# Kernel tuning notes

Measured on AMD Instinct MI355X. Metric: run time of the kernel, lower is better.

The kernel has to match this reference:

```python
import jax, jax.numpy as jnp
import numpy as np

N, E, G = 16384, 131072, 64
IN_DIM, HID, HEADS, GDIM, OUT_DIM = 256, 128, 4, 2, 2


def _glorot(key, shape):
    fan_in = shape[0]
    return jax.random.normal(key, shape, dtype=jnp.float32) / jnp.sqrt(jnp.float32(fan_in))


def gatv2_layer(x, src, dst, Wl, bl, Wr, br, att, bias, heads, ch, concat):
    """GATv2Conv: e_ij = att . leaky_relu(Wl x_j + Wr x_i, 0.2), segment softmax over dst."""
    n = x.shape[0]
    xl = (x @ Wl + bl).reshape(n, heads, ch)  # source transform
    xr = (x @ Wr + br).reshape(n, heads, ch)  # target transform
    h = jax.nn.leaky_relu(xl[src] + xr[dst], 0.2)          # [E', H, C]
    e = jnp.einsum('ehc,hc->eh', h, att)                   # [E', H]
    m = jax.ops.segment_max(e, dst, num_segments=n)        # stable softmax per target
    p = jnp.exp(e - m[dst])
    denom = jax.ops.segment_sum(p, dst, num_segments=n)
    alpha = p / denom[dst]                                 # self-loops guarantee denom>0
    out = jax.ops.segment_sum(alpha[..., None] * xl[src], dst, num_segments=n)  # [n,H,C]
    out = out.reshape(n, heads * ch) if concat else out.mean(axis=1)
    return out + bias


def setup_inputs() -> dict:
    key = jax.random.key(0)
    ks = jax.random.split(key, 24)
    inp = {
        'x': jax.random.normal(ks[0], (N, IN_DIM), dtype=jnp.float32),
        'edge_index': jax.random.randint(ks[1], (2, E), 0, N, dtype=jnp.int64)
            if jax.config.jax_enable_x64 else jax.random.randint(ks[1], (2, E), 0, N).astype(jnp.int32),
        'batch': jnp.sort(jax.random.randint(ks[2], (N,), 0, G)).astype(jnp.int32),
        'global_features': jax.random.normal(ks[3], (G, GDIM), dtype=jnp.float32),
    }
    # conv1: in=256 -> heads*hid=512 (concat)
    inp['c1_Wl'] = _glorot(ks[4], (IN_DIM, HEADS * HID)); inp['c1_bl'] = jnp.zeros((HEADS * HID,), jnp.float32)
    inp['c1_Wr'] = _glorot(ks[5], (IN_DIM, HEADS * HID)); inp['c1_br'] = jnp.zeros((HEADS * HID,), jnp.float32)
    inp['c1_att'] = _glorot(ks[6], (HEADS, HID)); inp['c1_bias'] = jnp.zeros((HEADS * HID,), jnp.float32)
    # conv2: in=512 -> 512 (concat)
    D2 = HEADS * HID
    inp['c2_Wl'] = _glorot(ks[7], (D2, HEADS * HID)); inp['c2_bl'] = jnp.zeros((HEADS * HID,), jnp.float32)
    inp['c2_Wr'] = _glorot(ks[8], (D2, HEADS * HID)); inp['c2_br'] = jnp.zeros((HEADS * HID,), jnp.float32)
    inp['c2_att'] = _glorot(ks[9], (HEADS, HID)); inp['c2_bias'] = jnp.zeros((HEADS * HID,), jnp.float32)
    # conv3: in=512 -> 128 (heads=1, concat=False)
    inp['c3_Wl'] = _glorot(ks[10], (D2, HID)); inp['c3_bl'] = jnp.zeros((HID,), jnp.float32)
    inp['c3_Wr'] = _glorot(ks[11], (D2, HID)); inp['c3_br'] = jnp.zeros((HID,), jnp.float32)
    inp['c3_att'] = _glorot(ks[12], (1, HID)); inp['c3_bias'] = jnp.zeros((HID,), jnp.float32)
    # classifier: (hid + global_dim) -> hid -> out
    inp['cls_W1'] = _glorot(ks[13], (HID + GDIM, HID)); inp['cls_b1'] = jnp.zeros((HID,), jnp.float32)
    inp['cls_W2'] = _glorot(ks[14], (HID, OUT_DIM)); inp['cls_b2'] = jnp.zeros((OUT_DIM,), jnp.float32)
    return inp


def reference(x, edge_index, batch, global_features,
              c1_Wl, c1_bl, c1_Wr, c1_br, c1_att, c1_bias,
              c2_Wl, c2_bl, c2_Wr, c2_br, c2_att, c2_bias,
              c3_Wl, c3_bl, c3_Wr, c3_br, c3_att, c3_bias,
              cls_W1, cls_b1, cls_W2, cls_b2):
    n = x.shape[0]
    # PyG GATv2Conv add_self_loops=True default
    loop = jnp.arange(n, dtype=edge_index.dtype)
    src = jnp.concatenate([edge_index[0], loop])
    dst = jnp.concatenate([edge_index[1], loop])

    h = jax.nn.leaky_relu(gatv2_layer(x, src, dst, c1_Wl, c1_bl, c1_Wr, c1_br, c1_att, c1_bias, HEADS, HID, True), 0.01)
    h = jax.nn.leaky_relu(gatv2_layer(h, src, dst, c2_Wl, c2_bl, c2_Wr, c2_br, c2_att, c2_bias, HEADS, HID, True), 0.01)
    h = jax.nn.leaky_relu(gatv2_layer(h, src, dst, c3_Wl, c3_bl, c3_Wr, c3_br, c3_att, c3_bias, 1, HID, False), 0.01)

    # global mean pool over graphs
    counts = jax.ops.segment_sum(jnp.ones((n,), h.dtype), batch, num_segments=G)
    pooled = jax.ops.segment_sum(h, batch, num_segments=G) / jnp.maximum(counts, 1.0)[:, None]

    z = jnp.concatenate([pooled, global_features.reshape(G, -1)], axis=-1)
    z = jax.nn.leaky_relu(z @ cls_W1 + cls_b1, 0.01)  # Dropout is identity at eval
    return z @ cls_W2 + cls_b2
```

## Files before the change

kernel.cpp:

```cpp
#include <hip/hip_runtime.h>

typedef _Float16 h16;
typedef _Float16 h16x2 __attribute__((ext_vector_type(2)));
typedef _Float16 h16x8 __attribute__((ext_vector_type(8)));
typedef float    f32x4 __attribute__((ext_vector_type(4)));

__device__ __forceinline__ void gload16(const h16* g, h16* l) {
    __builtin_amdgcn_global_load_lds(
        (const __attribute__((address_space(1))) void*)g,
        (__attribute__((address_space(3))) void*)l,
        16, 0, 0);
}

__global__ void prep(const float* __restrict__ Wl1, const float* __restrict__ Wr1,
                     const float* __restrict__ Wl2, const float* __restrict__ Wr2,
                     const float* __restrict__ Wl3, const float* __restrict__ Wr3,
                     h16* __restrict__ wt1, h16* __restrict__ wt2, h16* __restrict__ wt3,
                     const float* __restrict__ x, h16* __restrict__ xh,
                     int* __restrict__ deg, int* __restrict__ cursor,
                     const int* __restrict__ batch, int* __restrict__ start,
                     float* __restrict__ pooled, int Nn, int G)
{
    int i = blockIdx.x * blockDim.x + threadIdx.x;
    const int n_x = Nn * 32;
    if (i < n_x) {
        float4 a = *(const float4*)(x + (size_t)i * 8);
        float4 b = *(const float4*)(x + (size_t)i * 8 + 4);
        h16x8 o = { (h16)a.x, (h16)a.y, (h16)a.z, (h16)a.w,
                    (h16)b.x, (h16)b.y, (h16)b.z, (h16)b.w };
        *(h16x8*)(xh + (size_t)i * 8) = o;
        return;
    }
    i -= n_x;
    if (i < 131072) { int k = i >> 9, n = i & 511; wt1[n * 256 + k] = (h16)Wl1[i]; return; }
    i -= 131072;
    if (i < 131072) { int k = i >> 9, n = i & 511; wt1[512 * 256 + n * 256 + k] = (h16)Wr1[i]; return; }
    i -= 131072;
    if (i < 262144) { int k = i >> 9, n = i & 511; wt2[n * 512 + k] = (h16)Wl2[i]; return; }
    i -= 262144;
    if (i < 262144) { int k = i >> 9, n = i & 511; wt2[512 * 512 + n * 512 + k] = (h16)Wr2[i]; return; }
    i -= 262144;
    if (i < 65536)  { int k = i >> 7, n = i & 127; wt3[n * 512 + k] = (h16)Wl3[i]; return; }
    i -= 65536;
    if (i < 65536)  { int k = i >> 7, n = i & 127; wt3[128 * 512 + n * 512 + k] = (h16)Wr3[i]; return; }
    i -= 65536;
    if (i < Nn) { deg[i] = 0; return; }
    i -= Nn;
    if (i < Nn) { cursor[i] = 0; return; }
    i -= Nn;
    if (i < G * 128) { pooled[i] = 0.f; return; }
    i -= G * 128;
    if (i < Nn) {
        int b  = batch[i];
        int bp = (i == 0) ? -1 : batch[i - 1];
        for (int g = bp + 1; g <= b; g++) start[g] = i;
        if (i == Nn - 1) for (int g = b + 1; g <= G; g++) start[g] = Nn;
    }
}

__global__ void hist_dst(const int* __restrict__ ei, int E, int Nn, int* __restrict__ deg) {
    int i = blockIdx.x * blockDim.x + threadIdx.x;
    if (i >= E + Nn) return;
    int dst = (i < E) ? ei[E + i] : (i - E);
    atomicAdd(&deg[dst], 1);
}
__global__ __launch_bounds__(256) void scan16k(const int* __restrict__ deg, int* __restrict__ off, int Nn) {
    __shared__ int part[256];
    int t = threadIdx.x;
    const int4* d4 = (const int4*)deg;
    int s = 0;
    #pragma unroll
    for (int j = 0; j < 16; j++) { int4 q = d4[t * 16 + j]; s += q.x + q.y + q.z + q.w; }
    part[t] = s;
    __syncthreads();
    for (int d = 1; d < 256; d <<= 1) {
        int v = (t >= d) ? part[t - d] : 0;
        __syncthreads();
        part[t] += v;
        __syncthreads();
    }
    int run = (t > 0) ? part[t - 1] : 0;
    #pragma unroll
    for (int j = 0; j < 16; j++) {
        int4 q = d4[t * 16 + j];
        int4 o;
        o.x = run; run += q.x;
        o.y = run; run += q.y;
        o.z = run; run += q.z;
        o.w = run; run += q.w;
        ((int4*)off)[t * 16 + j] = o;
    }
}
__global__ void scatter_src(const int* __restrict__ ei, int E, int Nn,
                            const int* __restrict__ off, int* __restrict__ cursor,
                            int* __restrict__ ssrc) {
    int i = blockIdx.x * blockDim.x + threadIdx.x;
    if (i >= E + Nn) return;
    int src, dst;
    if (i < E) { src = ei[i]; dst = ei[E + i]; }
    else       { src = dst = i - E; }
    int p = atomicAdd(&cursor[dst], 1);
    ssrc[off[dst] + p] = src;
}

__global__ __launch_bounds__(512) void gemm_f16_wide(
    const h16* __restrict__ Xh, const h16* __restrict__ Wt,
    const float* __restrict__ bias_lo, const float* __restrict__ bias_hi, int nsplit,
    h16* __restrict__ Yl, h16* __restrict__ Yr, int M, int N, int K)
{
    __shared__ __align__(16) h16 As[2][128 * 64];
    __shared__ __align__(16) h16 Bs[2][256 * 64];

    const int m0 = blockIdx.y * 128;
    const int n0 = blockIdx.x * 256;
    const int t = threadIdx.x;
    const int lane = t & 63;
    const int wid = t >> 6;
    const int wr = wid >> 2;
    const int wc = wid & 3;

    f32x4 acc[4][4] = {};

    const int lr = lane >> 3;
    const int sl = lane & 7;

    #define STAGE(b, k0)                                                          \
        _Pragma("unroll")                                                         \
        for (int q = 0; q < 6; q++) {                                             \
            int rb = wid + 8 * q;                      \
            if (rb < 16) {                                                        \
                int r = rb * 8 + lr;                                              \
                int col = (sl ^ (r & 7)) << 3;                                    \
                gload16(Xh + (size_t)(m0 + r) * K + (k0) + col, &As[b][rb * 8 * 64]); \
            } else {                                                              \
                int c = (rb - 16) * 8 + lr;                                       \
                int col = (sl ^ (c & 7)) << 3;                                    \
                gload16(Wt + (size_t)(n0 + c) * K + (k0) + col, &Bs[b][(rb - 16) * 8 * 64]); \
            }                                                                     \
        }

    STAGE(0, 0)
    __syncthreads();

    const int nkb = K >> 6;
    int buf = 0;
    for (int kb = 0; kb < nkb; kb++) {
        if (kb + 1 < nkb) { STAGE(buf ^ 1, (kb + 1) << 6) }
        #pragma unroll
        for (int ks = 0; ks < 2; ks++) {
            h16x8 af[4], bf[4];
            #pragma unroll
            for (int i = 0; i < 4; i++) {
                int r  = wr * 64 + i * 16 + (lane & 15);
                int s2 = ks * 4 + (lane >> 4);
                af[i] = *(const h16x8*)(&As[buf][r * 64 + ((s2 ^ (r & 7)) << 3)]);
                int c  = wc * 64 + i * 16 + (lane & 15);
                bf[i] = *(const h16x8*)(&Bs[buf][c * 64 + ((s2 ^ (c & 7)) << 3)]);
            }
            #pragma unroll
            for (int i = 0; i < 4; i++)
                #pragma unroll
                for (int j = 0; j < 4; j++)
                    acc[i][j] = __builtin_amdgcn_mfma_f32_16x16x32_f16(af[i], bf[j], acc[i][j], 0, 0, 0);
        }
        __syncthreads();
        buf ^= 1;
    }
    #undef STAGE

    const int crow = (lane >> 4) * 4;
    const int ccol = lane & 15;
    #pragma unroll
    for (int i = 0; i < 4; i++) {
        int rg = m0 + wr * 64 + i * 16 + crow;
        #pragma unroll
        for (int j = 0; j < 4; j++) {
            int cg = n0 + wc * 64 + j * 16 + ccol;
            float b = (cg < nsplit) ? bias_lo[cg] : bias_hi[cg - nsplit];
            h16* dst = (cg < nsplit) ? (Yl + (size_t)cg) : (Yr + (size_t)(cg - nsplit));
            #pragma unroll
            for (int rr = 0; rr < 4; rr++)
                dst[(size_t)(rg + rr) * nsplit] = (h16)(acc[i][j][rr] + b);
        }
    }
}

__global__ __launch_bounds__(256) void gemm_f16_mfma(
    const h16* __restrict__ Xh, const h16* __restrict__ Wt,
    const float* __restrict__ bias_lo, const float* __restrict__ bias_hi, int nsplit,
    h16* __restrict__ Yl, h16* __restrict__ Yr, int M, int N, int K)
{
    __shared__ __align__(16) h16 As[2][128 * 64];
    __shared__ __align__(16) h16 Bs[2][128 * 64];

    const int m0 = blockIdx.y * 128;
    const int n0 = blockIdx.x * 128;
    const int t = threadIdx.x;
    const int lane = t & 63;
    const int wid = t >> 6;
    const int wr = wid >> 1, wc = wid & 1;

    f32x4 acc[4][4] = {};

    const int rA = wid * 32;
    const int lr = lane >> 3;
    const int sl = lane & 7;

    #define STAGE(b, k0)                                                        \
        _Pragma("unroll")                                                       \
        for (int q = 0; q < 4; q++) {                                           \
            int rb = rA + q * 8;                                                \
            int r  = rb + lr;                                                   \
            int col = (sl ^ (r & 7)) << 3;                                      \
            gload16(Xh + (size_t)(m0 + r) * K + (k0) + col, &As[b][rb * 64]);   \
            gload16(Wt + (size_t)(n0 + r) * K + (k0) + col, &Bs[b][rb * 64]);   \
        }

    STAGE(0, 0)
    __syncthreads();

    const int nkb = K >> 6;
    int buf = 0;
    for (int kb = 0; kb < nkb; kb++) {
        if (kb + 1 < nkb) { STAGE(buf ^ 1, (kb + 1) << 6) }
        #pragma unroll
        for (int ks = 0; ks < 2; ks++) {
            h16x8 af[4], bf[4];
            #pragma unroll
            for (int i = 0; i < 4; i++) {
                int r  = wr * 64 + i * 16 + (lane & 15);
                int s2 = ks * 4 + (lane >> 4);
                af[i] = *(const h16x8*)(&As[buf][r * 64 + ((s2 ^ (r & 7)) << 3)]);
                int c  = wc * 64 + i * 16 + (lane & 15);
                bf[i] = *(const h16x8*)(&Bs[buf][c * 64 + ((s2 ^ (c & 7)) << 3)]);
            }
            #pragma unroll
            for (int i = 0; i < 4; i++)
                #pragma unroll
                for (int j = 0; j < 4; j++)
                    acc[i][j] = __builtin_amdgcn_mfma_f32_16x16x32_f16(af[i], bf[j], acc[i][j], 0, 0, 0);
        }
        __syncthreads();
        buf ^= 1;
    }
    #undef STAGE

    const int crow = (lane >> 4) * 4;
    const int ccol = lane & 15;
    #pragma unroll
    for (int i = 0; i < 4; i++) {
        int rg = m0 + wr * 64 + i * 16 + crow;
        #pragma unroll
        for (int j = 0; j < 4; j++) {
            int cg = n0 + wc * 64 + j * 16 + ccol;
            float b = (cg < nsplit) ? bias_lo[cg] : bias_hi[cg - nsplit];
            h16* dst = (cg < nsplit) ? (Yl + (size_t)cg) : (Yr + (size_t)(cg - nsplit));
            #pragma unroll
            for (int rr = 0; rr < 4; rr++)
                dst[(size_t)(rg + rr) * nsplit] = (h16)(acc[i][j][rr] + b);
        }
    }
}

template<int H, int C, bool OUT16>
__global__ __launch_bounds__(256) void node_attn(
    const h16* __restrict__ xl, const h16* __restrict__ xr,
    const float* __restrict__ att, const float* __restrict__ bias,
    const int* __restrict__ off, const int* __restrict__ deg,
    const int* __restrict__ ssrc,
    void* __restrict__ out_v, int Nn)
{
    constexpr int D   = H * C;
    constexpr int EPL = D / 64;
    constexpr int LPH = C / EPL;
    int node = blockIdx.x * (blockDim.x >> 6) + (threadIdx.x >> 6);
    if (node >= Nn) return;
    const int lane = threadIdx.x & 63;
    const int base = lane * EPL;

    float xrv[EPL], attv[EPL];
    {
        const h16* pr = xr + (size_t)node * D + base;
        if constexpr (EPL == 8) {
            h16x8 v = *(const h16x8*)pr;
            float4 a0 = *(const float4*)(att + base);
            float4 a1 = *(const float4*)(att + base + 4);
            #pragma unroll
            for (int j = 0; j < 8; j++) xrv[j] = (float)v[j];
            attv[0] = a0.x; attv[1] = a0.y; attv[2] = a0.z; attv[3] = a0.w;
            attv[4] = a1.x; attv[5] = a1.y; attv[6] = a1.z; attv[7] = a1.w;
        } else {
            #pragma unroll
            for (int j = 0; j < EPL; j++) { xrv[j] = (float)pr[j]; attv[j] = att[base + j]; }
        }
    }

    float m = -INFINITY, denom = 0.f;
    float agg[EPL] = {};

    auto loadrow = [&](int src, float* xv) {
        const h16* pl = xl + (size_t)src * D + base;
        if constexpr (EPL == 8) {
            h16x8 v = *(const h16x8*)pl;
            #pragma unroll
            for (int j = 0; j < 8; j++) xv[j] = (float)v[j];
        } else {
            h16x2 v = *(const h16x2*)pl;
            #pragma unroll
            for (int j = 0; j < EPL; j++) xv[j] = (float)v[j];
        }
    };
    auto score = [&](const float* xv) {
        float s = 0.f;
        #pragma unroll
        for (int j = 0; j < EPL; j++) {
            float v = xv[j] + xrv[j];
            v = v > 0.f ? v : 0.2f * v;
            s += v * attv[j];
        }
        return s;
    };
    auto update = [&](float s, const float* xv) {
        if (s > m) {
            float scale = __expf(m - s);
            denom *= scale;
            #pragma unroll
            for (int j = 0; j < EPL; j++) agg[j] *= scale;
            m = s;
        }
        float p = __expf(s - m);
        denom += p;
        #pragma unroll
        for (int j = 0; j < EPL; j++) agg[j] += p * xv[j];
    };

    const int e0 = off[node], e1 = e0 + deg[node];
    int e = e0;
    for (; e + 3 < e1; e += 4) {
        int sA = ssrc[e], sB = ssrc[e + 1], sC = ssrc[e + 2], sD = ssrc[e + 3];
        float xa[EPL], xb[EPL], xc[EPL], xd[EPL];
        loadrow(sA, xa); loadrow(sB, xb); loadrow(sC, xc); loadrow(sD, xd);
        float s0 = score(xa), s1 = score(xb), s2 = score(xc), s3 = score(xd);
        #pragma unroll
        for (int o = 1; o < LPH; o <<= 1) {
            s0 += __shfl_xor(s0, o, 64);
            s1 += __shfl_xor(s1, o, 64);
            s2 += __shfl_xor(s2, o, 64);
            s3 += __shfl_xor(s3, o, 64);
        }
        update(s0, xa); update(s1, xb); update(s2, xc); update(s3, xd);
    }
    for (; e + 1 < e1; e += 2) {
        int sA = ssrc[e], sB = ssrc[e + 1];
        float xa[EPL], xb[EPL];
        loadrow(sA, xa); loadrow(sB, xb);
        float s0 = score(xa), s1 = score(xb);
        #pragma unroll
        for (int o = 1; o < LPH; o <<= 1) {
            s0 += __shfl_xor(s0, o, 64);
            s1 += __shfl_xor(s1, o, 64);
        }
        update(s0, xa); update(s1, xb);
    }
    if (e < e1) {
        int sA = ssrc[e];
        float xa[EPL];
        loadrow(sA, xa);
        float s0 = score(xa);
        #pragma unroll
        for (int o = 1; o < LPH; o <<= 1) s0 += __shfl_xor(s0, o, 64);
        update(s0, xa);
    }

    if constexpr (OUT16) {
        h16* po = (h16*)out_v + (size_t)node * D + base;
        if constexpr (EPL == 8) {
            h16x8 o8;
            #pragma unroll
            for (int j = 0; j < 8; j++) {
                float v = agg[j] / denom + bias[base + j];
                o8[j] = (h16)(v > 0.f ? v : 0.01f * v);
            }
            *(h16x8*)po = o8;
        } else {
            #pragma unroll
            for (int j = 0; j < EPL; j++) {
                float v = agg[j] / denom + bias[base + j];
                po[j] = (h16)(v > 0.f ? v : 0.01f * v);
            }
        }
    } else {
        float* po = (float*)out_v + (size_t)node * D + base;
        #pragma unroll
        for (int j = 0; j < EPL; j++) {
            float v = agg[j] / denom + bias[base + j];
            po[j] = v > 0.f ? v : 0.01f * v;
        }
    }
}

__global__ __launch_bounds__(128) void pool_partial(
    const float* __restrict__ h, const int* __restrict__ batch,
    float* __restrict__ pooled, int Nn, int spb)
{
    int t = threadIdx.x;
    int n0 = blockIdx.x * spb;
    int n1 = min(n0 + spb, Nn);
    if (n0 >= n1) return;
    int cur = batch[n0];
    float acc = 0.f;
    for (int n = n0; n < n1; n++) {
        int g = batch[n];
        if (g != cur) {
            atomicAdd(&pooled[cur * 128 + t], acc);
            acc = 0.f; cur = g;
        }
        acc += h[(size_t)n * 128 + t];
    }
    atomicAdd(&pooled[cur * 128 + t], acc);
}

__global__ __launch_bounds__(128) void classifier(
    const float* __restrict__ pooled, const int* __restrict__ start,
    const float* __restrict__ gf,
    const float* __restrict__ W1, const float* __restrict__ b1,
    const float* __restrict__ W2, const float* __restrict__ b2,
    float* __restrict__ out)
{
    __shared__ float z[130];
    __shared__ float hid[128];
    int g = blockIdx.x, t = threadIdx.x;
    float cnt = fmaxf((float)(start[g + 1] - start[g]), 1.f);
    z[t] = pooled[g * 128 + t] / cnt;
    if (t < 2) z[128 + t] = gf[g * 2 + t];
    __syncthreads();
    float s = b1[t];
    for (int k = 0; k < 130; k++) s += z[k] * W1[k * 128 + t];
    hid[t] = s > 0.f ? s : 0.01f * s;
    __syncthreads();
    if (t < 2) {
        float o = b2[t];
        for (int j = 0; j < 128; j++) o += hid[j] * W2[j * 2 + t];
        out[g * 2 + t] = o;
    }
}

static inline int cdiv(int a, int b) { return (a + b - 1) / b; }

extern "C" void kernel_launch(void* const* d_in, const int* in_sizes, int n_in,
                              void* d_out, int out_size, void* d_ws, size_t ws_size,
                              hipStream_t stream)
{
    const float* x     = (const float*)d_in[0];
    const int*   ei    = (const int*)d_in[1];
    const int*   batch = (const int*)d_in[2];
    const float* gf    = (const float*)d_in[3];

    const float* c_Wl[3]   = {(const float*)d_in[4],  (const float*)d_in[10], (const float*)d_in[16]};
    const float* c_bl[3]   = {(const float*)d_in[5],  (const float*)d_in[11], (const float*)d_in[17]};
    const float* c_Wr[3]   = {(const float*)d_in[6],  (const float*)d_in[12], (const float*)d_in[18]};
    const float* c_br[3]   = {(const float*)d_in[7],  (const float*)d_in[13], (const float*)d_in[19]};
    const float* c_att[3]  = {(const float*)d_in[8],  (const float*)d_in[14], (const float*)d_in[20]};
    const float* c_bias[3] = {(const float*)d_in[9],  (const float*)d_in[15], (const float*)d_in[21]};
    const float* W1 = (const float*)d_in[22];
    const float* b1 = (const float*)d_in[23];
    const float* W2 = (const float*)d_in[24];
    const float* b2 = (const float*)d_in[25];
    float* out = (float*)d_out;

    const int Nn   = in_sizes[0] / 256;
    const int E    = in_sizes[1] / 2;
    const int G    = in_sizes[3] / 2;
    const int Etot = E + Nn;

    char* w = (char*)d_ws;
    auto carve = [&](size_t bytes) { void* p = w; w += (bytes + 255) & ~(size_t)255; return p; };
    h16*   ylb  = (h16*)carve((size_t)Nn * 512 * 2);
    h16*   yrb  = (h16*)carve((size_t)Nn * 512 * 2);
    h16*   xh   = (h16*)carve((size_t)Nn * 512 * 2);
    float* b0   = (float*)carve((size_t)Nn * 128 * 4);
    h16* wt1 = (h16*)carve((size_t)1024 * 256 * 2);
    h16* wt2 = (h16*)carve((size_t)1024 * 512 * 2);
    h16* wt3 = (h16*)carve((size_t)256 * 512 * 2);
    int* deg    = (int*)carve((size_t)Nn * 4);
    int* off    = (int*)carve((size_t)Nn * 4);
    int* cursor = (int*)carve((size_t)Nn * 4);
    int* ssrc   = (int*)carve((size_t)Etot * 4);
    int* start  = (int*)carve((size_t)(G + 1) * 4);
    float* pooled = (float*)carve((size_t)G * 128 * 4);
    (void)ws_size; (void)n_in; (void)out_size;

    {
        const int total = Nn * 32 + 131072 * 2 + 262144 * 2 + 65536 * 2
                        + Nn * 2 + G * 128 + Nn;
        prep<<<cdiv(total, 256), 256, 0, stream>>>(c_Wl[0], c_Wr[0], c_Wl[1], c_Wr[1],
                                                   c_Wl[2], c_Wr[2], wt1, wt2, wt3,
                                                   x, xh, deg, cursor, batch, start,
                                                   pooled, Nn, G);
    }
    hist_dst<<<cdiv(Etot, 256), 256, 0, stream>>>(ei, E, Nn, deg);
    scan16k<<<1, 256, 0, stream>>>(deg, off, Nn);
    scatter_src<<<cdiv(Etot, 256), 256, 0, stream>>>(ei, E, Nn, off, cursor, ssrc);

    const int node_blocks = cdiv(Nn, 4);

    gemm_f16_wide<<<dim3(1024 / 256, Nn / 128), 512, 0, stream>>>(xh, wt1, c_bl[0], c_br[0], 512, ylb, yrb, Nn, 1024, 256);
    node_attn<4, 128, true><<<node_blocks, 256, 0, stream>>>(ylb, yrb, c_att[0], c_bias[0], off, deg, ssrc, xh, Nn);
    gemm_f16_wide<<<dim3(1024 / 256, Nn / 128), 512, 0, stream>>>(xh, wt2, c_bl[1], c_br[1], 512, ylb, yrb, Nn, 1024, 512);
    node_attn<4, 128, true><<<node_blocks, 256, 0, stream>>>(ylb, yrb, c_att[1], c_bias[1], off, deg, ssrc, xh, Nn);
    gemm_f16_mfma<<<dim3(256 / 128, Nn / 128), 256, 0, stream>>>(xh, wt3, c_bl[2], c_br[2], 128, ylb, yrb, Nn, 256, 512);
    node_attn<1, 128, false><<<node_blocks, 256, 0, stream>>>(ylb, yrb, c_att[2], c_bias[2], off, deg, ssrc, b0, Nn);

    {
        const int nblk = 256;
        const int spb  = cdiv(Nn, nblk);
        pool_partial<<<nblk, 128, 0, stream>>>(b0, batch, pooled, Nn, spb);
    }
    classifier<<<G, 128, 0, stream>>>(pooled, start, gf, W1, b1, W2, b2, out);
}
```

Measured before the change: 208.7 us.

## Tile weight transposes via LDS, remap GEMM blocks per XCD, specialize single-head attention

Moves the fp32-to-fp16 weight transpose out of the per-element prep kernel into a separate kernel that uses 32x32 LDS tiles, so both the reads and the writes are coalesced. Both GEMMs now remap the block index so that consecutive M tiles land on the same XCD, which is meant to improve L2 reuse of the shared weight tiles. The single-head third attention layer gets its own kernel that splits each wavefront into four 16-lane groups, each handling different edges with 8-wide fp16 loads, and merges their online-softmax states with cross-lane shuffles. The risks are one extra kernel launch and the assumption that gridDim.y is divisible by 8.

```diff
diff --git a/kernel.cpp b/kernel.cpp
--- a/kernel.cpp
+++ b/kernel.cpp
@@ -12,11 +12,40 @@
         16, 0, 0);
 }
 
-__global__ void prep(const float* __restrict__ Wl1, const float* __restrict__ Wr1,
-                     const float* __restrict__ Wl2, const float* __restrict__ Wr2,
-                     const float* __restrict__ Wl3, const float* __restrict__ Wr3,
-                     h16* __restrict__ wt1, h16* __restrict__ wt2, h16* __restrict__ wt3,
-                     const float* __restrict__ x, h16* __restrict__ xh,
+__global__ __launch_bounds__(256) void wtrans(
+    const float* __restrict__ W0, const float* __restrict__ W1,
+    const float* __restrict__ W2, const float* __restrict__ W3,
+    const float* __restrict__ W4, const float* __restrict__ W5,
+    h16* __restrict__ O0, h16* __restrict__ O1, h16* __restrict__ O2,
+    h16* __restrict__ O3, h16* __restrict__ O4, h16* __restrict__ O5)
+{
+    __shared__ float lds[32][33];
+    const int mtx = blockIdx.y;
+    const float* Ws[6] = {W0, W1, W2, W3, W4, W5};
+    h16*         Os[6] = {O0, O1, O2, O3, O4, O5};
+    const int    Ks[6] = {256, 256, 512, 512, 512, 512};
+    const int    Ns[6] = {512, 512, 512, 512, 128, 128};
+    const float* W = Ws[mtx];
+    h16*         O = Os[mtx];
+    const int K = Ks[mtx], N = Ns[mtx];
+    const int ntiles = (K >> 5) * (N >> 5);
+    const int tile = blockIdx.x;
+    if (tile >= ntiles) return;
+    const int tk = tile / (N >> 5), tn = tile % (N >> 5);
+    const int t = threadIdx.x;
+    const int r = t >> 3, c4 = (t & 7) * 4;
+
+    float4 v = *(const float4*)(W + (size_t)(tk * 32 + r) * N + tn * 32 + c4);
+    lds[r][c4] = v.x; lds[r][c4 + 1] = v.y; lds[r][c4 + 2] = v.z; lds[r][c4 + 3] = v.w;
+    __syncthreads();
+    h16* po = O + (size_t)(tn * 32 + r) * K + tk * 32 + c4;
+    po[0] = (h16)lds[c4 + 0][r];
+    po[1] = (h16)lds[c4 + 1][r];
+    po[2] = (h16)lds[c4 + 2][r];
+    po[3] = (h16)lds[c4 + 3][r];
+}
+
+__global__ void prep(const float* __restrict__ x, h16* __restrict__ xh,
                      int* __restrict__ deg, int* __restrict__ cursor,
                      const int* __restrict__ batch, int* __restrict__ start,
                      float* __restrict__ pooled, int Nn, int G)
@@ -32,18 +61,6 @@
         return;
     }
     i -= n_x;
-    if (i < 131072) { int k = i >> 9, n = i & 511; wt1[n * 256 + k] = (h16)Wl1[i]; return; }
-    i -= 131072;
-    if (i < 131072) { int k = i >> 9, n = i & 511; wt1[512 * 256 + n * 256 + k] = (h16)Wr1[i]; return; }
-    i -= 131072;
-    if (i < 262144) { int k = i >> 9, n = i & 511; wt2[n * 512 + k] = (h16)Wl2[i]; return; }
-    i -= 262144;
-    if (i < 262144) { int k = i >> 9, n = i & 511; wt2[512 * 512 + n * 512 + k] = (h16)Wr2[i]; return; }
-    i -= 262144;
-    if (i < 65536)  { int k = i >> 7, n = i & 127; wt3[n * 512 + k] = (h16)Wl3[i]; return; }
-    i -= 65536;
-    if (i < 65536)  { int k = i >> 7, n = i & 127; wt3[128 * 512 + n * 512 + k] = (h16)Wr3[i]; return; }
-    i -= 65536;
     if (i < Nn) { deg[i] = 0; return; }
     i -= Nn;
     if (i < Nn) { cursor[i] = 0; return; }
@@ -103,6 +120,13 @@
     ssrc[off[dst] + p] = src;
 }
 
+__device__ __forceinline__ void xcd_tiles(int& mt, int& nt) {
+    int d = blockIdx.x + blockIdx.y * gridDim.x;
+    int k = d & 7, j = d >> 3;
+    mt = k * (gridDim.y >> 3) + j / gridDim.x;
+    nt = j % gridDim.x;
+}
+
 __global__ __launch_bounds__(512) void gemm_f16_wide(
     const h16* __restrict__ Xh, const h16* __restrict__ Wt,
     const float* __restrict__ bias_lo, const float* __restrict__ bias_hi, int nsplit,
@@ -111,8 +135,10 @@
     __shared__ __align__(16) h16 As[2][128 * 64];
     __shared__ __align__(16) h16 Bs[2][256 * 64];
 
-    const int m0 = blockIdx.y * 128;
-    const int n0 = blockIdx.x * 256;
+    int mt, nt;
+    xcd_tiles(mt, nt);
+    const int m0 = mt * 128;
+    const int n0 = nt * 256;
     const int t = threadIdx.x;
     const int lane = t & 63;
     const int wid = t >> 6;
@@ -193,8 +219,10 @@
     __shared__ __align__(16) h16 As[2][128 * 64];
     __shared__ __align__(16) h16 Bs[2][128 * 64];
 
-    const int m0 = blockIdx.y * 128;
-    const int n0 = blockIdx.x * 128;
+    int mt, nt;
+    xcd_tiles(mt, nt);
+    const int m0 = mt * 128;
+    const int n0 = nt * 128;
     const int t = threadIdx.x;
     const int lane = t & 63;
     const int wid = t >> 6;
@@ -262,13 +290,13 @@
     }
 }
 
-template<int H, int C, bool OUT16>
+template<int H, int C>
 __global__ __launch_bounds__(256) void node_attn(
     const h16* __restrict__ xl, const h16* __restrict__ xr,
     const float* __restrict__ att, const float* __restrict__ bias,
     const int* __restrict__ off, const int* __restrict__ deg,
     const int* __restrict__ ssrc,
-    void* __restrict__ out_v, int Nn)
+    h16* __restrict__ out, int Nn)
 {
     constexpr int D   = H * C;
     constexpr int EPL = D / 64;
@@ -281,34 +309,22 @@
     float xrv[EPL], attv[EPL];
     {
         const h16* pr = xr + (size_t)node * D + base;
-        if constexpr (EPL == 8) {
-            h16x8 v = *(const h16x8*)pr;
-            float4 a0 = *(const float4*)(att + base);
-            float4 a1 = *(const float4*)(att + base + 4);
-            #pragma unroll
-            for (int j = 0; j < 8; j++) xrv[j] = (float)v[j];
-            attv[0] = a0.x; attv[1] = a0.y; attv[2] = a0.z; attv[3] = a0.w;
-            attv[4] = a1.x; attv[5] = a1.y; attv[6] = a1.z; attv[7] = a1.w;
-        } else {
-            #pragma unroll
-            for (int j = 0; j < EPL; j++) { xrv[j] = (float)pr[j]; attv[j] = att[base + j]; }
-        }
+        h16x8 v = *(const h16x8*)pr;
+        float4 a0 = *(const float4*)(att + base);
+        float4 a1 = *(const float4*)(att + base + 4);
+        #pragma unroll
+        for (int j = 0; j < 8; j++) xrv[j] = (float)v[j];
+        attv[0] = a0.x; attv[1] = a0.y; attv[2] = a0.z; attv[3] = a0.w;
+        attv[4] = a1.x; attv[5] = a1.y; attv[6] = a1.z; attv[7] = a1.w;
     }
 
     float m = -INFINITY, denom = 0.f;
     float agg[EPL] = {};
 
     auto loadrow = [&](int src, float* xv) {
-        const h16* pl = xl + (size_t)src * D + base;
-        if constexpr (EPL == 8) {
-            h16x8 v = *(const h16x8*)pl;
-            #pragma unroll
-            for (int j = 0; j < 8; j++) xv[j] = (float)v[j];
-        } else {
-            h16x2 v = *(const h16x2*)pl;
-            #pragma unroll
-            for (int j = 0; j < EPL; j++) xv[j] = (float)v[j];
-        }
+        h16x8 v = *(const h16x8*)(xl + (size_t)src * D + base);
+        #pragma unroll
+        for (int j = 0; j < 8; j++) xv[j] = (float)v[j];
     };
     auto score = [&](const float* xv) {
         float s = 0.f;
@@ -372,27 +388,92 @@
         update(s0, xa);
     }
 
-    if constexpr (OUT16) {
-        h16* po = (h16*)out_v + (size_t)node * D + base;
-        if constexpr (EPL == 8) {
-            h16x8 o8;
-            #pragma unroll
-            for (int j = 0; j < 8; j++) {
-                float v = agg[j] / denom + bias[base + j];
-                o8[j] = (h16)(v > 0.f ? v : 0.01f * v);
-            }
-            *(h16x8*)po = o8;
-        } else {
-            #pragma unroll
-            for (int j = 0; j < EPL; j++) {
-                float v = agg[j] / denom + bias[base + j];
-                po[j] = (h16)(v > 0.f ? v : 0.01f * v);
-            }
-        }
-    } else {
-        float* po = (float*)out_v + (size_t)node * D + base;
-        #pragma unroll
-        for (int j = 0; j < EPL; j++) {
+    h16* po = out + (size_t)node * D + base;
+    h16x8 o8;
+    #pragma unroll
+    for (int j = 0; j < 8; j++) {
+        float v = agg[j] / denom + bias[base + j];
+        o8[j] = (h16)(v > 0.f ? v : 0.01f * v);
+    }
+    *(h16x8*)po = o8;
+}
+
+__global__ __launch_bounds__(256) void node_attn_h1(
+    const h16* __restrict__ xl, const h16* __restrict__ xr,
+    const float* __restrict__ att, const float* __restrict__ bias,
+    const int* __restrict__ off, const int* __restrict__ deg,
+    const int* __restrict__ ssrc,
+    float* __restrict__ out, int Nn)
+{
+    int node = blockIdx.x * 4 + (threadIdx.x >> 6);
+    if (node >= Nn) return;
+    const int lane = threadIdx.x & 63;
+    const int q    = lane >> 4;
+    const int sl   = lane & 15;
+    const int base = sl * 8;
+
+    float xrv[8], attv[8];
+    {
+        h16x8 v = *(const h16x8*)(xr + (size_t)node * 128 + base);
+        float4 a0 = *(const float4*)(att + base);
+        float4 a1 = *(const float4*)(att + base + 4);
+        #pragma unroll
+        for (int j = 0; j < 8; j++) xrv[j] = (float)v[j];
+        attv[0] = a0.x; attv[1] = a0.y; attv[2] = a0.z; attv[3] = a0.w;
+        attv[4] = a1.x; attv[5] = a1.y; attv[6] = a1.z; attv[7] = a1.w;
+    }
+
+    float m = -1e30f, denom = 0.f;
+    float agg[8] = {};
+
+    const int e0 = off[node], e1 = e0 + deg[node];
+    for (int e = e0 + q; e < e1; e += 4) {
+        int src = ssrc[e];
+        h16x8 v = *(const h16x8*)(xl + (size_t)src * 128 + base);
+        float xv[8];
+        #pragma unroll
+        for (int j = 0; j < 8; j++) xv[j] = (float)v[j];
+        float s = 0.f;
+        #pragma unroll
+        for (int j = 0; j < 8; j++) {
+            float u = xv[j] + xrv[j];
+            u = u > 0.f ? u : 0.2f * u;
+            s += u * attv[j];
+        }
+        #pragma unroll
+        for (int o = 1; o < 16; o <<= 1) s += __shfl_xor(s, o, 64);
+        if (s > m) {
+            float sc = __expf(m - s);
+            denom *= sc;
+            #pragma unroll
+            for (int j = 0; j < 8; j++) agg[j] *= sc;
+            m = s;
+        }
+        float p = __expf(s - m);
+        denom += p;
+        #pragma unroll
+        for (int j = 0; j < 8; j++) agg[j] += p * xv[j];
+    }
+
+    #pragma unroll
+    for (int o = 16; o <= 32; o <<= 1) {
+        float m2 = __shfl_xor(m, o, 64);
+        float d2 = __shfl_xor(denom, o, 64);
+        float a2[8];
+        #pragma unroll
+        for (int j = 0; j < 8; j++) a2[j] = __shfl_xor(agg[j], o, 64);
+        float mn = fmaxf(m, m2);
+        float sa = __expf(m - mn), sb = __expf(m2 - mn);
+        denom = denom * sa + d2 * sb;
+        #pragma unroll
+        for (int j = 0; j < 8; j++) agg[j] = agg[j] * sa + a2[j] * sb;
+        m = mn;
+    }
+
+    if (lane < 16) {
+        float* po = out + (size_t)node * 128 + base;
+        #pragma unroll
+        for (int j = 0; j < 8; j++) {
             float v = agg[j] / denom + bias[base + j];
             po[j] = v > 0.f ? v : 0.01f * v;
         }
@@ -491,12 +572,14 @@
     (void)ws_size; (void)n_in; (void)out_size;
 
     {
-        const int total = Nn * 32 + 131072 * 2 + 262144 * 2 + 65536 * 2
-                        + Nn * 2 + G * 128 + Nn;
-        prep<<<cdiv(total, 256), 256, 0, stream>>>(c_Wl[0], c_Wr[0], c_Wl[1], c_Wr[1],
-                                                   c_Wl[2], c_Wr[2], wt1, wt2, wt3,
-                                                   x, xh, deg, cursor, batch, start,
+        const int total = Nn * 32 + Nn * 2 + G * 128 + Nn;
+        prep<<<cdiv(total, 256), 256, 0, stream>>>(x, xh, deg, cursor, batch, start,
                                                    pooled, Nn, G);
+        wtrans<<<dim3(256, 6), 256, 0, stream>>>(c_Wl[0], c_Wr[0], c_Wl[1], c_Wr[1],
+                                                 c_Wl[2], c_Wr[2],
+                                                 wt1, wt1 + 512 * 256,
+                                                 wt2, wt2 + 512 * 512,
+                                                 wt3, wt3 + 128 * 512);
     }
     hist_dst<<<cdiv(Etot, 256), 256, 0, stream>>>(ei, E, Nn, deg);
     scan16k<<<1, 256, 0, stream>>>(deg, off, Nn);
@@ -505,11 +588,11 @@
     const int node_blocks = cdiv(Nn, 4);
 
     gemm_f16_wide<<<dim3(1024 / 256, Nn / 128), 512, 0, stream>>>(xh, wt1, c_bl[0], c_br[0], 512, ylb, yrb, Nn, 1024, 256);
-    node_attn<4, 128, true><<<node_blocks, 256, 0, stream>>>(ylb, yrb, c_att[0], c_bias[0], off, deg, ssrc, xh, Nn);
+    node_attn<4, 128><<<node_blocks, 256, 0, stream>>>(ylb, yrb, c_att[0], c_bias[0], off, deg, ssrc, xh, Nn);
     gemm_f16_wide<<<dim3(1024 / 256, Nn / 128), 512, 0, stream>>>(xh, wt2, c_bl[1], c_br[1], 512, ylb, yrb, Nn, 1024, 512);
-    node_attn<4, 128, true><<<node_blocks, 256, 0, stream>>>(ylb, yrb, c_att[1], c_bias[1], off, deg, ssrc, xh, Nn);
+    node_attn<4, 128><<<node_blocks, 256, 0, stream>>>(ylb, yrb, c_att[1], c_bias[1], off, deg, ssrc, xh, Nn);
     gemm_f16_mfma<<<dim3(256 / 128, Nn / 128), 256, 0, stream>>>(xh, wt3, c_bl[2], c_br[2], 128, ylb, yrb, Nn, 256, 512);
-    node_attn<1, 128, false><<<node_blocks, 256, 0, stream>>>(ylb, yrb, c_att[2], c_bias[2], off, deg, ssrc, b0, Nn);
+    node_attn_h1<<<node_blocks, 256, 0, stream>>>(ylb, yrb, c_att[2], c_bias[2], off, deg, ssrc, b0, Nn);
 
     {
         const int nblk = 256;
```

Result: faster. 202.9 us (-2.8%).
